# Optimization experiments

Measured on AMD Instinct MI355X. Metric: run time of the kernel, lower is better.

The kernel has to match this reference:

```python
import jax, jax.numpy as jnp
import numpy as np

RADIUS = 0.1
NSAMPLE = 32
NUM_KP = 15
KP_EXTENT = 1.0
DENSITY_PARAM = 5.0
EXTENT = 2.0 * KP_EXTENT * RADIUS / DENSITY_PARAM  # 0.04
K_RADIUS = 1.5 * EXTENT                            # 0.06
C_IN, C_OUT = 64, 128
BN_EPS = 1e-5


def make_kernel_points():
    # Deterministic stand-in for create_kernel_points: first point at center
    # ('center' fixed mode), remaining points quasi-uniform in a ball of K_RADIUS.
    rs = np.random.RandomState(0)
    d = rs.randn(NUM_KP - 1, 3)
    d /= np.linalg.norm(d, axis=1, keepdims=True) + 1e-9
    r = rs.rand(NUM_KP - 1, 1) ** (1.0 / 3.0)
    pts = np.concatenate([np.zeros((1, 3)), d * r * K_RADIUS], axis=0)
    return jnp.asarray(pts, dtype=jnp.float32)  # [K, 3]


def ball_group(query_xyz, support_xyz, support_mask, radius, nsample):
    """Masked ordered ball query. Returns idx [B,N1,S] int32 and mask [B,N1,S] float."""
    # [B, N1, N2] squared distances (dominant memory traffic)
    d2 = jnp.sum((query_xyz[:, :, None, :] - support_xyz[:, None, :, :]) ** 2, axis=-1)
    valid = (d2 < radius * radius) & (support_mask[:, None, :] > 0)
    order = jnp.cumsum(valid.astype(jnp.int32), axis=-1) - 1  # rank among valid, per row
    in_cap = valid & (order < nsample)
    slot = jnp.where(in_cap, order, nsample)  # overflow -> dump slot
    B, N1, N2 = d2.shape
    j = jnp.broadcast_to(jnp.arange(N2, dtype=jnp.int32), (B, N1, N2))
    b = jnp.arange(B)[:, None, None]
    n = jnp.arange(N1)[None, :, None]
    idx = jnp.zeros((B, N1, nsample + 1), jnp.int32).at[b, n, slot].set(j)[..., :nsample]
    cnt = jnp.sum(in_cap.astype(jnp.int32), axis=-1)  # [B, N1]
    nb_mask = jnp.arange(nsample)[None, None, :] < cnt[:, :, None]
    idx = jnp.where(nb_mask, idx, idx[:, :, :1])  # pad with first neighbor
    return idx, nb_mask.astype(jnp.float32)


def setup_inputs() -> dict:
    key = jax.random.key(0)
    ks = jax.random.split(key, 6)
    B, N1, N2 = 4, 2048, 8192
    query_xyz = jax.random.uniform(ks[0], (B, N1, 3), dtype=jnp.float32)
    support_xyz = jax.random.uniform(ks[1], (B, N2, 3), dtype=jnp.float32)
    query_mask = jnp.ones((B, N1), jnp.float32)
    support_mask = jnp.ones((B, N2), jnp.float32)
    support_features = jax.random.normal(ks[2], (B, C_IN, N2), dtype=jnp.float32)
    kernel_weights = jax.random.normal(ks[3], (NUM_KP, C_IN), dtype=jnp.float32) * (1.0 / np.sqrt(C_IN))
    W_out = jax.random.normal(ks[4], (C_OUT, C_IN), dtype=jnp.float32) * (1.0 / np.sqrt(C_IN))
    gamma = jnp.ones((C_OUT,), jnp.float32)
    beta = jnp.zeros((C_OUT,), jnp.float32)
    return {
        "query_xyz": query_xyz, "support_xyz": support_xyz,
        "query_mask": query_mask, "support_mask": support_mask,
        "support_features": support_features, "K_points": make_kernel_points(),
        "kernel_weights": kernel_weights, "W_out": W_out,
        "gamma": gamma, "beta": beta,
    }


def reference(query_xyz, support_xyz, query_mask, support_mask, support_features,
              K_points, kernel_weights, W_out, gamma, beta):
    idx, nb_mask = ball_group(query_xyz, support_xyz, support_mask, RADIUS, NSAMPLE)
    # gather neighbor features: [B, N2, C] -> [B, N1, S, C]
    feats_t = jnp.transpose(support_features, (0, 2, 1))
    nbr_feats = jnp.take_along_axis(feats_t[:, None, :, :],
                                    idx[:, :, :, None], axis=2)  # [B,N1,S,C]
    # grouped relative positions: [B, N1, S, 3]
    grouped_xyz = jnp.take_along_axis(support_xyz[:, None, :, :],
                                      idx[:, :, :, None], axis=2)
    rel_pos = grouped_xyz - query_xyz[:, :, None, :]
    # kernel-point distances: [B, N1, S, K]
    diff = rel_pos[:, :, :, None, :] - K_points[None, None, None, :, :]
    sq_d = jnp.sum(diff * diff, axis=-1)
    # linear influence, then permute to [B, N1, K, S]
    w = jnp.clip(1.0 - jnp.sqrt(sq_d) / EXTENT, 0.0, None)
    w = jnp.transpose(w, (0, 1, 3, 2))
    feature_mask = nb_mask + (1.0 - query_mask[:, :, None])  # [B,N1,S]
    w = w * feature_mask[:, :, None, :]
    # weighted sum over neighbors: [B, N1, K, C]
    weighted = jnp.einsum('bnks,bnsc->bnkc', w, nbr_feats)
    out = jnp.sum(weighted * kernel_weights[None, None, :, :], axis=2)  # [B,N1,C]
    out = jnp.transpose(out, (0, 2, 1))  # [B, C_in, N1]
    # out_conv: 1x1 conv (no bias) + BatchNorm1d (training-mode batch stats) + ReLU
    out = jnp.einsum('oc,bcn->bon', W_out, out)  # [B, C_out, N1]
    mean = jnp.mean(out, axis=(0, 2), keepdims=True)
    var = jnp.mean((out - mean) ** 2, axis=(0, 2), keepdims=True)
    out = (out - mean) * jax.lax.rsqrt(var + BN_EPS)
    out = out * gamma[None, :, None] + beta[None, :, None]
    return jax.nn.relu(out)
```

## Files before the change

kernel.cpp:

```cpp
#include <hip/hip_runtime.h>
#include <stdint.h>
#include <limits.h>

#define BATCH 4
#define N1D   2048
#define N2D   8192
#define NSAMP 32
#define NKP   15
#define CIN   64
#define COUT  128

#define RAD2    0.01f
#define INV_EXT 25.0f
#define BN_EPS  1e-5f
#define CMARG   0.1000001f

#define QPW   1
#define NWAVE 4
#define QPB   (QPW*NWAVE)
#define NCELL 1000
#define MAXC  96

#define WS_PTS4   0
#define WS_BPTS   131072
#define WS_FEATT  262144
#define WS_WT     2359296
#define WS_OUT2   2367488
#define WS_CS     3416064
#define WS_CNT    3420160
#define WS_CUR    3424256

__device__ __forceinline__ int cell_of(float x, float y, float z) {
  int cx = (int)(x*10.f); cx = cx < 0 ? 0 : (cx > 9 ? 9 : cx);
  int cy = (int)(y*10.f); cy = cy < 0 ? 0 : (cy > 9 ? 9 : cy);
  int cz = (int)(z*10.f); cz = cz < 0 ? 0 : (cz > 9 ? 9 : cz);
  return (cx*10 + cy)*10 + cz;
}

__global__ __launch_bounds__(256) void pg_prep(
    const float* __restrict__ sxyz, const float* __restrict__ smask,
    const float* __restrict__ sfeat, const float* __restrict__ Wout,
    float4* __restrict__ pts4, float* __restrict__ featT, float* __restrict__ Wt,
    int* __restrict__ cellCnt)
{
  __shared__ float tile[64*65];
  const int t  = threadIdx.x;
  const int bt = blockIdx.x;

  if (bt == 512) {
#pragma unroll
    for (int i = 0; i < 32; ++i) {
      const int flat = i*256 + t;
      Wt[flat] = Wout[(flat & 127)*CIN + (flat >> 7)];
    }
    return;
  }

  if (bt >= 513) {
    const int idx = bt - 513;
    const int bb  = idx >> 5;
    const int i   = ((idx & 31) << 8) + t;
    if (smask[bb*N2D + i] > 0.f) {
      const float* p = sxyz + ((size_t)bb*N2D + i)*3;
      atomicAdd(&cellCnt[bb*1024 + cell_of(p[0], p[1], p[2])], 1);
    }
    return;
  }

  const int b  = bt >> 7;
  const int j0 = (bt & 127) * 64;
  if (t < 64) {
    const int g = bt*64 + t;
    pts4[g] = make_float4(sxyz[g*3+0], sxyz[g*3+1], sxyz[g*3+2], 0.f);
  }
  const float* src = sfeat + (size_t)(b*CIN)*N2D + j0;
#pragma unroll
  for (int i = 0; i < 4; ++i) {
    const int c  = i*16 + (t >> 4);
    const int j4 = (t & 15) * 4;
    const float4 v = *(const float4*)(src + (size_t)c*N2D + j4);
    tile[c*65 + j4+0] = v.x;
    tile[c*65 + j4+1] = v.y;
    tile[c*65 + j4+2] = v.z;
    tile[c*65 + j4+3] = v.w;
  }
  __syncthreads();
  float* dstb = featT + (size_t)(b*N2D + j0) * CIN;
#pragma unroll
  for (int r = 0; r < 4; ++r) {
    const int j  = r*16 + (t >> 4);
    const int c4 = (t & 15) * 4;
    float4 v;
    v.x = tile[(c4+0)*65 + j];
    v.y = tile[(c4+1)*65 + j];
    v.z = tile[(c4+2)*65 + j];
    v.w = tile[(c4+3)*65 + j];
    *(float4*)(dstb + j*CIN + c4) = v;
  }
}

__global__ __launch_bounds__(256) void pg_scan(
    const int* __restrict__ cellCnt, int* __restrict__ cellStart,
    int* __restrict__ cellCur)
{
  __shared__ int off_s[NCELL+1];
  __shared__ int wsum[4];
  const int t    = threadIdx.x;
  const int lane = t & 63;
  const int wv   = t >> 6;
  const int bb   = blockIdx.x;
  const int* cnt = cellCnt + bb*1024;

  int c0 = 0, c1 = 0, c2 = 0, c3 = 0, v = 0;
  if (t < 250) {
    c0 = cnt[t*4+0]; c1 = cnt[t*4+1]; c2 = cnt[t*4+2]; c3 = cnt[t*4+3];
    v = c0 + c1 + c2 + c3;
  }
  int x = v;
#pragma unroll
  for (int off = 1; off < 64; off <<= 1) {
    int y = __shfl_up(x, off);
    if (lane >= off) x += y;
  }
  if (lane == 63) wsum[wv] = x;
  __syncthreads();
  int base = 0;
#pragma unroll
  for (int w = 0; w < 4; ++w) if (w < wv) base += wsum[w];
  const int excl = base + x - v;
  if (t < 250) {
    int o = excl;
    off_s[t*4+0] = o; o += c0;
    off_s[t*4+1] = o; o += c1;
    off_s[t*4+2] = o; o += c2;
    off_s[t*4+3] = o;
  }
  if (t == 0) off_s[NCELL] = wsum[0]+wsum[1]+wsum[2]+wsum[3];
  __syncthreads();
  for (int i = t; i < NCELL; i += 256) {
    const int o = off_s[i];
    cellStart[bb*(NCELL+1) + i] = o;
    cellCur[bb*1024 + i] = o;
  }
  if (t == 0) cellStart[bb*(NCELL+1) + NCELL] = off_s[NCELL];
}

__global__ __launch_bounds__(256) void pg_scatter(
    const float* __restrict__ sxyz, const float* __restrict__ smask,
    int* __restrict__ cellCur, float4* __restrict__ bpts)
{
  const int idx = blockIdx.x;
  const int bb  = idx >> 5;
  const int i   = ((idx & 31) << 8) + threadIdx.x;
  if (smask[bb*N2D + i] > 0.f) {
    const float* p = sxyz + ((size_t)bb*N2D + i)*3;
    const float px = p[0], py = p[1], pz = p[2];
    const int pos = atomicAdd(&cellCur[bb*1024 + cell_of(px,py,pz)], 1);
    bpts[(size_t)bb*N2D + pos] = make_float4(px, py, pz, __int_as_float(i));
  }
}

__global__ __launch_bounds__(256) void pg_main(
    const float* __restrict__ qxyz, const float* __restrict__ qmask,
    const float4* __restrict__ pts4, const float4* __restrict__ bpts,
    const int* __restrict__ cellStart, const float* __restrict__ featT,
    const float* __restrict__ Kp, const float* __restrict__ KW,
    const float* __restrict__ Wt, float* __restrict__ out2)
{
  __shared__ int      s_segb[QPB][12];
  __shared__ int      s_segc[QPB][12];
  __shared__ int      s_cand[QPB][MAXC];
  __shared__ int      s_idx[QPB*NSAMP];
  __shared__ int      s_cnt[QPB];
  __shared__ float    s_w[QPB*NSAMP*17];
  __shared__ unsigned s_wm[QPB*NSAMP];
  __shared__ float    s_xq[QPB*65];

  const int t    = threadIdx.x;
  const int lane = t & 63;
  const int wv   = t >> 6;
  const int gbase = blockIdx.x * QPB;
  const int b     = gbase >> 11;
  const uint64_t lt = (1ull << lane) - 1ull;

  const float4* bptsb = bpts + (size_t)b*N2D;
  {
    const int ql = wv;
    const int g  = gbase + ql;
    const float qx = qxyz[g*3+0], qy = qxyz[g*3+1], qz = qxyz[g*3+2];
    int cx0 = (int)((qx-CMARG)*10.f); if (cx0 < 0) cx0 = 0;
    int cx1 = (int)((qx+CMARG)*10.f); if (cx1 > 9) cx1 = 9;
    int cy0 = (int)((qy-CMARG)*10.f); if (cy0 < 0) cy0 = 0;
    int cy1 = (int)((qy+CMARG)*10.f); if (cy1 > 9) cy1 = 9;
    int cz0 = (int)((qz-CMARG)*10.f); if (cz0 < 0) cz0 = 0;
    int cz1 = (int)((qz+CMARG)*10.f); if (cz1 > 9) cz1 = 9;
    const int ny = cy1 - cy0 + 1;
    const int npair = (cx1 - cx0 + 1) * ny;

    int len = 0, rs = 0;
    if (lane < npair) {
      const int cx = cx0 + lane / ny;
      const int cy = cy0 + lane % ny;
      const int rowb = (cx*10 + cy)*10;
      const int* csb = cellStart + b*(NCELL+1) + rowb;
      rs = csb[cz0];
      len = csb[cz1 + 1] - rs;
    }
    int c = len;
#pragma unroll
    for (int off = 1; off < 16; off <<= 1) {
      int y = __shfl_up(c, off);
      if (lane >= off) c += y;
    }
    const int tot = __shfl(c, 15);
    const int excl = c - len;
    if (lane < npair) s_segb[ql][lane] = rs - excl;
    if (lane <= npair) s_segc[ql][lane] = excl;

    int ccnt = 0;
    for (int base = 0; base < tot; base += 64) {
      const int idx = base + lane;
      bool ok = false; int jj = 0;
      if (idx < tot) {
        int p = 0;
        while (s_segc[ql][p+1] <= idx) ++p;
        const float4 pt = bptsb[s_segb[ql][p] + idx];
        const float dx = pt.x - qx, dy = pt.y - qy, dz = pt.z - qz;
        ok = (dx*dx + dy*dy + dz*dz) < RAD2;
        jj = __float_as_int(pt.w);
      }
      const uint64_t m = __ballot(ok);
      if (ok) {
        const int pos = ccnt + __popcll(m & lt);
        if (pos < MAXC) s_cand[ql][pos] = jj;
      }
      ccnt += (int)__popcll(m);
    }
    const int C = ccnt < MAXC ? ccnt : MAXC;
    const int C4 = (C + 3) & ~3;
    if (C + lane < C4) s_cand[ql][C + lane] = INT_MAX;

    int jA = (lane      < C) ? s_cand[ql][lane]      : INT_MAX;
    int jB = (lane + 64 < C) ? s_cand[ql][lane + 64] : INT_MAX;
    int rA = 0, rB = 0;
    for (int e = 0; e < C4; e += 4) {
      const int4 v4 = *(const int4*)&s_cand[ql][e];
      rA += (v4.x < jA) + (v4.y < jA) + (v4.z < jA) + (v4.w < jA);
      rB += (v4.x < jB) + (v4.y < jB) + (v4.z < jB) + (v4.w < jB);
    }
    if (lane      < C && rA < NSAMP) s_idx[ql*NSAMP + rA] = jA;
    if (lane + 64 < C && rB < NSAMP) s_idx[ql*NSAMP + rB] = jB;
    if (lane == 0) s_cnt[ql] = C < NSAMP ? C : NSAMP;
  }
  __syncthreads();

  if (t < QPB*NSAMP) {
    const int qslot = t >> 5;
    const int s = t & 31;
    const int c = s_cnt[qslot];
    int j;
    if (s < c) {
      j = s_idx[t];
    } else {
      j = (c > 0) ? s_idx[qslot*NSAMP] : 0;
      s_idx[t] = j;
    }
    const int g = gbase + qslot;
    const float4 pj = pts4[b*N2D + j];
    const float rx = pj.x - qxyz[g*3+0];
    const float ry = pj.y - qxyz[g*3+1];
    const float rz = pj.z - qxyz[g*3+2];

    unsigned msk = 0u;
#pragma unroll
    for (int k = 0; k < NKP; ++k) {
      const float dx = rx - Kp[k*3+0];
      const float dy = ry - Kp[k*3+1];
      const float dz = rz - Kp[k*3+2];
      const float dd = dx*dx + dy*dy + dz*dz;
      const float w = 1.0f - sqrtf(dd) * INV_EXT;
      if (w > 0.0f) {
        s_w[t*17 + k] = w;
        msk |= (1u << k);
      }
    }
    s_wm[t] = msk;
  }
  __syncthreads();

  float kw[NKP];
#pragma unroll
  for (int k = 0; k < NKP; ++k) kw[k] = KW[k*CIN + lane];

  {
    const int ql = wv;
    const int g = gbase + ql;
    const float fpad = 1.0f - qmask[g];
    const int c = __builtin_amdgcn_readfirstlane(s_cnt[ql]);

    float ft[NSAMP];
#pragma unroll
    for (int s = 0; s < NSAMP; ++s) {
      const int j = __builtin_amdgcn_readfirstlane(s_idx[ql*NSAMP + s]);
      ft[s] = featT[(size_t)(b*N2D + j)*CIN + lane];
    }

    float acc = 0.0f;
#pragma unroll
    for (int s = 0; s < NSAMP; ++s) {
      const float fm = ((s < c) ? 1.0f : 0.0f) + fpad;
      if (fm != 0.0f) {
        const unsigned mk =
            (unsigned)__builtin_amdgcn_readfirstlane((int)s_wm[ql*NSAMP + s]);
        if (mk != 0u) {
          const float* wp = &s_w[(ql*NSAMP + s)*17];
          float wsum = 0.0f;
#pragma unroll
          for (int k = 0; k < NKP; ++k)
            if (mk & (1u << k)) wsum += wp[k] * kw[k];
          acc = fmaf(fm*wsum, ft[s], acc);
        }
      }
    }
    s_xq[ql*65 + lane] = acc;
  }
  __syncthreads();

  {
    const int n4 = t & 3;
    const int og = t >> 2;
    const int g  = gbase + n4;
    const int nn = g & 2047;
    float a0 = 0.f, a1 = 0.f;
#pragma unroll
    for (int c = 0; c < CIN; ++c) {
      const float xc = s_xq[n4*65 + c];
      const float2 w2 = *(const float2*)(Wt + c*COUT + og*2);
      a0 = fmaf(w2.x, xc, a0);
      a1 = fmaf(w2.y, xc, a1);
    }
    float* ob = out2 + (size_t)(b*COUT + og*2)*N1D + nn;
    ob[0]   = a0;
    ob[N1D] = a1;
  }
}

__global__ __launch_bounds__(256) void pg_finish(
    const float* __restrict__ out2, const float* __restrict__ gamma,
    const float* __restrict__ beta, float* __restrict__ dout)
{
  __shared__ float red[8];
  __shared__ float mv[2];
  const int t  = threadIdx.x;
  const int o  = blockIdx.x & 127;
  const int bb = blockIdx.x >> 7;
  float4 f[4][2];
  float s1 = 0.f, s2 = 0.f;
#pragma unroll
  for (int r = 0; r < BATCH; ++r) {
    const float4* p = (const float4*)(out2 + (size_t)(r*COUT + o)*N1D);
#pragma unroll
    for (int i = 0; i < 2; ++i) {
      const float4 x = p[i*256 + t];
      f[r][i] = x;
      s1 += x.x + x.y + x.z + x.w;
      s2 += x.x*x.x + x.y*x.y + x.z*x.z + x.w*x.w;
    }
  }
#pragma unroll
  for (int off = 32; off; off >>= 1) {
    s1 += __shfl_xor(s1, off);
    s2 += __shfl_xor(s2, off);
  }
  const int wv = t >> 6;
  if ((t & 63) == 0) { red[wv] = s1; red[4+wv] = s2; }
  __syncthreads();
  if (t == 0) {
    const float inv = 1.0f / (float)(BATCH*N1D);
    const float mean = (red[0]+red[1]+red[2]+red[3]) * inv;
    const float var  = (red[4]+red[5]+red[6]+red[7]) * inv - mean*mean;
    mv[0] = mean;
    mv[1] = rsqrtf(var + BN_EPS);
  }
  __syncthreads();
  const float mean = mv[0];
  const float ga = gamma[o] * mv[1];
  const float be = beta[o];
  float4* dp = (float4*)(dout + (size_t)(bb*COUT + o)*N1D);
#pragma unroll
  for (int i = 0; i < 2; ++i) {
    const float4 x = f[bb][i];
    float4 y;
    y.x = fmaxf((x.x - mean)*ga + be, 0.0f);
    y.y = fmaxf((x.y - mean)*ga + be, 0.0f);
    y.z = fmaxf((x.z - mean)*ga + be, 0.0f);
    y.w = fmaxf((x.w - mean)*ga + be, 0.0f);
    dp[i*256 + t] = y;
  }
}

extern "C" void kernel_launch(void* const* d_in, const int* in_sizes, int n_in,
                              void* d_out, int out_size, void* d_ws, size_t ws_size,
                              hipStream_t stream)
{
  const float* qxyz  = (const float*)d_in[0];
  const float* sxyz  = (const float*)d_in[1];
  const float* qmask = (const float*)d_in[2];
  const float* smask = (const float*)d_in[3];
  const float* sfeat = (const float*)d_in[4];
  const float* Kp    = (const float*)d_in[5];
  const float* KW    = (const float*)d_in[6];
  const float* Wout  = (const float*)d_in[7];
  const float* gamma = (const float*)d_in[8];
  const float* beta  = (const float*)d_in[9];
  float* ws = (float*)d_ws;
  float4* pts4 = (float4*)(ws + WS_PTS4);
  float4* bpts = (float4*)(ws + WS_BPTS);
  float* featT = ws + WS_FEATT;
  float* Wt    = ws + WS_WT;
  float* out2  = ws + WS_OUT2;
  int*   cellS = (int*)(ws + WS_CS);
  int*   cellC = (int*)(ws + WS_CNT);
  int*   cellU = (int*)(ws + WS_CUR);
  float* dst   = (float*)d_out;

  hipMemsetAsync(cellC, 0, BATCH*1024*sizeof(int), stream);
  pg_prep   <<<641,  256, 0, stream>>>(sxyz, smask, sfeat, Wout, pts4, featT,
                                       Wt, cellC);
  pg_scan   <<<4,    256, 0, stream>>>(cellC, cellS, cellU);
  pg_scatter<<<128,  256, 0, stream>>>(sxyz, smask, cellU, bpts);
  pg_main   <<<2048, 256, 0, stream>>>(qxyz, qmask, pts4, bpts, cellS, featT,
                                       Kp, KW, Wt, out2);
  pg_finish <<<512,  256, 0, stream>>>(out2, gamma, beta, dst);
}
```

Before: 144.9 us.

## Make pg_main wave-local, drop block barriers and Wout transpose

Each wave now handles its own query end to end: segment tables live in registers via readlane, and kernel-point weights are computed by the same wave, split across two half-waves. This removes two __syncthreads and the shared count arrays. The separate Wout transpose block in pg_prep is dropped, and the 1x1 conv reads Wout rows directly with float4 loads over padded shared rows. The main risks are higher register pressure and uncoalesced Wout row reads in the conv stage.

```diff
diff --git a/kernel.cpp b/kernel.cpp
--- a/kernel.cpp
+++ b/kernel.cpp
@@ -15,16 +15,14 @@
 #define BN_EPS  1e-5f
 #define CMARG   0.1000001f
 
-#define QPW   1
 #define NWAVE 4
-#define QPB   (QPW*NWAVE)
+#define QPB   NWAVE
 #define NCELL 1000
 #define MAXC  96
 
 #define WS_PTS4   0
 #define WS_BPTS   131072
 #define WS_FEATT  262144
-#define WS_WT     2359296
 #define WS_OUT2   2367488
 #define WS_CS     3416064
 #define WS_CNT    3420160
@@ -39,25 +37,15 @@
 
 __global__ __launch_bounds__(256) void pg_prep(
     const float* __restrict__ sxyz, const float* __restrict__ smask,
-    const float* __restrict__ sfeat, const float* __restrict__ Wout,
-    float4* __restrict__ pts4, float* __restrict__ featT, float* __restrict__ Wt,
-    int* __restrict__ cellCnt)
+    const float* __restrict__ sfeat, float4* __restrict__ pts4,
+    float* __restrict__ featT, int* __restrict__ cellCnt)
 {
   __shared__ float tile[64*65];
   const int t  = threadIdx.x;
   const int bt = blockIdx.x;
 
-  if (bt == 512) {
-#pragma unroll
-    for (int i = 0; i < 32; ++i) {
-      const int flat = i*256 + t;
-      Wt[flat] = Wout[(flat & 127)*CIN + (flat >> 7)];
-    }
-    return;
-  }
-
-  if (bt >= 513) {
-    const int idx = bt - 513;
+  if (bt >= 512) {
+    const int idx = bt - 512;
     const int bb  = idx >> 5;
     const int i   = ((idx & 31) << 8) + t;
     if (smask[bb*N2D + i] > 0.f) {
@@ -165,16 +153,12 @@
     const float4* __restrict__ pts4, const float4* __restrict__ bpts,
     const int* __restrict__ cellStart, const float* __restrict__ featT,
     const float* __restrict__ Kp, const float* __restrict__ KW,
-    const float* __restrict__ Wt, float* __restrict__ out2)
-{
-  __shared__ int      s_segb[QPB][12];
-  __shared__ int      s_segc[QPB][12];
-  __shared__ int      s_cand[QPB][MAXC];
-  __shared__ int      s_idx[QPB*NSAMP];
-  __shared__ int      s_cnt[QPB];
-  __shared__ float    s_w[QPB*NSAMP*17];
-  __shared__ unsigned s_wm[QPB*NSAMP];
-  __shared__ float    s_xq[QPB*65];
+    const float* __restrict__ Wout, float* __restrict__ out2)
+{
+  __shared__ __align__(16) int  s_cand[QPB][MAXC];
+  __shared__ int2               s_im[QPB][NSAMP];
+  __shared__ float              s_w[QPB*NSAMP*17];
+  __shared__ float              s_xq[QPB*68];
 
   const int t    = threadIdx.x;
   const int lane = t & 63;
@@ -183,11 +167,12 @@
   const int b     = gbase >> 11;
   const uint64_t lt = (1ull << lane) - 1ull;
 
+  const int g = gbase + wv;
+  const float qx = qxyz[g*3+0], qy = qxyz[g*3+1], qz = qxyz[g*3+2];
+
   const float4* bptsb = bpts + (size_t)b*N2D;
+  int cq;
   {
-    const int ql = wv;
-    const int g  = gbase + ql;
-    const float qx = qxyz[g*3+0], qy = qxyz[g*3+1], qz = qxyz[g*3+2];
     int cx0 = (int)((qx-CMARG)*10.f); if (cx0 < 0) cx0 = 0;
     int cx1 = (int)((qx+CMARG)*10.f); if (cx1 > 9) cx1 = 9;
     int cy0 = (int)((qy-CMARG)*10.f); if (cy0 < 0) cy0 = 0;
@@ -201,30 +186,38 @@
     if (lane < npair) {
       const int cx = cx0 + lane / ny;
       const int cy = cy0 + lane % ny;
-      const int rowb = (cx*10 + cy)*10;
-      const int* csb = cellStart + b*(NCELL+1) + rowb;
-      rs = csb[cz0];
+      const int* csb = cellStart + b*(NCELL+1) + (cx*10 + cy)*10;
+      rs  = csb[cz0];
       len = csb[cz1 + 1] - rs;
     }
-    int c = len;
+    int pc = len;
 #pragma unroll
     for (int off = 1; off < 16; off <<= 1) {
-      int y = __shfl_up(c, off);
-      if (lane >= off) c += y;
-    }
-    const int tot = __shfl(c, 15);
-    const int excl = c - len;
-    if (lane < npair) s_segb[ql][lane] = rs - excl;
-    if (lane <= npair) s_segc[ql][lane] = excl;
+      int y = __shfl_up(pc, off);
+      if (lane >= off) pc += y;
+    }
+    const int tot   = __shfl(pc, 15);
+    const int excl  = pc - len;
+    const int sbase = rs - excl;
+
+    int segc[9], segb[9];
+#pragma unroll
+    for (int e = 0; e < 9; ++e) {
+      const int ce = __builtin_amdgcn_readlane(excl,  e);
+      const int be = __builtin_amdgcn_readlane(sbase, e);
+      segc[e] = (e < npair) ? ce : INT_MAX;
+      segb[e] = (e < npair) ? be : 0;
+    }
 
     int ccnt = 0;
-    for (int base = 0; base < tot; base += 64) {
-      const int idx = base + lane;
+    for (int base0 = 0; base0 < tot; base0 += 64) {
+      const int idx = base0 + lane;
       bool ok = false; int jj = 0;
       if (idx < tot) {
-        int p = 0;
-        while (s_segc[ql][p+1] <= idx) ++p;
-        const float4 pt = bptsb[s_segb[ql][p] + idx];
+        int bb2 = segb[0];
+#pragma unroll
+        for (int e = 1; e < 9; ++e) if (segc[e] <= idx) bb2 = segb[e];
+        const float4 pt = bptsb[bb2 + idx];
         const float dx = pt.x - qx, dy = pt.y - qy, dz = pt.z - qz;
         ok = (dx*dx + dy*dy + dz*dz) < RAD2;
         jj = __float_as_int(pt.w);
@@ -232,88 +225,84 @@
       const uint64_t m = __ballot(ok);
       if (ok) {
         const int pos = ccnt + __popcll(m & lt);
-        if (pos < MAXC) s_cand[ql][pos] = jj;
+        if (pos < MAXC) s_cand[wv][pos] = jj;
       }
       ccnt += (int)__popcll(m);
     }
     const int C = ccnt < MAXC ? ccnt : MAXC;
     const int C4 = (C + 3) & ~3;
-    if (C + lane < C4) s_cand[ql][C + lane] = INT_MAX;
-
-    int jA = (lane      < C) ? s_cand[ql][lane]      : INT_MAX;
-    int jB = (lane + 64 < C) ? s_cand[ql][lane + 64] : INT_MAX;
+    if (C + lane < C4) s_cand[wv][C + lane] = INT_MAX;
+
+    int jA = (lane      < C) ? s_cand[wv][lane]      : INT_MAX;
+    int jB = (lane + 64 < C) ? s_cand[wv][lane + 64] : INT_MAX;
     int rA = 0, rB = 0;
     for (int e = 0; e < C4; e += 4) {
-      const int4 v4 = *(const int4*)&s_cand[ql][e];
+      const int4 v4 = *(const int4*)&s_cand[wv][e];
       rA += (v4.x < jA) + (v4.y < jA) + (v4.z < jA) + (v4.w < jA);
       rB += (v4.x < jB) + (v4.y < jB) + (v4.z < jB) + (v4.w < jB);
     }
-    if (lane      < C && rA < NSAMP) s_idx[ql*NSAMP + rA] = jA;
-    if (lane + 64 < C && rB < NSAMP) s_idx[ql*NSAMP + rB] = jB;
-    if (lane == 0) s_cnt[ql] = C < NSAMP ? C : NSAMP;
-  }
-  __syncthreads();
-
-  if (t < QPB*NSAMP) {
-    const int qslot = t >> 5;
-    const int s = t & 31;
-    const int c = s_cnt[qslot];
-    int j;
-    if (s < c) {
-      j = s_idx[t];
-    } else {
-      j = (c > 0) ? s_idx[qslot*NSAMP] : 0;
-      s_idx[t] = j;
-    }
-    const int g = gbase + qslot;
+    if (lane      < C && rA < NSAMP) s_im[wv][rA].x = jA;
+    if (lane + 64 < C && rB < NSAMP) s_im[wv][rB].x = jB;
+    cq = C < NSAMP ? C : NSAMP;
+  }
+
+  {
+    const int s    = lane & 31;
+    const int half = lane >> 5;
+    const int raw  = s_im[wv][s].x;
+    const int r0   = s_im[wv][0].x;
+    const int j = (s < cq) ? raw : (cq > 0 ? r0 : 0);
+    if (half == 0) s_im[wv][s].x = j;
+
     const float4 pj = pts4[b*N2D + j];
-    const float rx = pj.x - qxyz[g*3+0];
-    const float ry = pj.y - qxyz[g*3+1];
-    const float rz = pj.z - qxyz[g*3+2];
+    const float rx = pj.x - qx;
+    const float ry = pj.y - qy;
+    const float rz = pj.z - qz;
 
     unsigned msk = 0u;
 #pragma unroll
-    for (int k = 0; k < NKP; ++k) {
-      const float dx = rx - Kp[k*3+0];
-      const float dy = ry - Kp[k*3+1];
-      const float dz = rz - Kp[k*3+2];
-      const float dd = dx*dx + dy*dy + dz*dz;
-      const float w = 1.0f - sqrtf(dd) * INV_EXT;
-      if (w > 0.0f) {
-        s_w[t*17 + k] = w;
-        msk |= (1u << k);
+    for (int ki = 0; ki < 8; ++ki) {
+      const int k = half*8 + ki;
+      if (k < NKP) {
+        const float dx = rx - Kp[k*3+0];
+        const float dy = ry - Kp[k*3+1];
+        const float dz = rz - Kp[k*3+2];
+        const float dd = dx*dx + dy*dy + dz*dz;
+        const float w = 1.0f - sqrtf(dd) * INV_EXT;
+        if (w > 0.0f) {
+          s_w[(wv*NSAMP + s)*17 + k] = w;
+          msk |= (1u << k);
+        }
       }
     }
-    s_wm[t] = msk;
-  }
-  __syncthreads();
-
-  float kw[NKP];
-#pragma unroll
-  for (int k = 0; k < NKP; ++k) kw[k] = KW[k*CIN + lane];
+    msk |= (unsigned)__shfl_xor((int)msk, 32);
+    if (half == 0) s_im[wv][s].y = (int)msk;
+  }
 
   {
-    const int ql = wv;
-    const int g = gbase + ql;
+    float kw[NKP];
+#pragma unroll
+    for (int k = 0; k < NKP; ++k) kw[k] = KW[k*CIN + lane];
+
     const float fpad = 1.0f - qmask[g];
-    const int c = __builtin_amdgcn_readfirstlane(s_cnt[ql]);
+    const int cqs = __builtin_amdgcn_readfirstlane(cq);
 
     float ft[NSAMP];
 #pragma unroll
     for (int s = 0; s < NSAMP; ++s) {
-      const int j = __builtin_amdgcn_readfirstlane(s_idx[ql*NSAMP + s]);
+      const int j = __builtin_amdgcn_readfirstlane(s_im[wv][s].x);
       ft[s] = featT[(size_t)(b*N2D + j)*CIN + lane];
     }
 
     float acc = 0.0f;
 #pragma unroll
     for (int s = 0; s < NSAMP; ++s) {
-      const float fm = ((s < c) ? 1.0f : 0.0f) + fpad;
+      const float fm = ((s < cqs) ? 1.0f : 0.0f) + fpad;
       if (fm != 0.0f) {
         const unsigned mk =
-            (unsigned)__builtin_amdgcn_readfirstlane((int)s_wm[ql*NSAMP + s]);
+            (unsigned)__builtin_amdgcn_readfirstlane(s_im[wv][s].y);
         if (mk != 0u) {
-          const float* wp = &s_w[(ql*NSAMP + s)*17];
+          const float* wp = &s_w[(wv*NSAMP + s)*17];
           float wsum = 0.0f;
 #pragma unroll
           for (int k = 0; k < NKP; ++k)
@@ -322,22 +311,26 @@
         }
       }
     }
-    s_xq[ql*65 + lane] = acc;
+    s_xq[wv*68 + lane] = acc;
   }
   __syncthreads();
 
   {
     const int n4 = t & 3;
     const int og = t >> 2;
-    const int g  = gbase + n4;
-    const int nn = g & 2047;
+    const int gq = gbase + n4;
+    const int nn = gq & 2047;
+    const float4* xr = (const float4*)&s_xq[n4*68];
+    const float4* w0 = (const float4*)(Wout + (og*2+0)*CIN);
+    const float4* w1 = (const float4*)(Wout + (og*2+1)*CIN);
     float a0 = 0.f, a1 = 0.f;
 #pragma unroll
-    for (int c = 0; c < CIN; ++c) {
-      const float xc = s_xq[n4*65 + c];
-      const float2 w2 = *(const float2*)(Wt + c*COUT + og*2);
-      a0 = fmaf(w2.x, xc, a0);
-      a1 = fmaf(w2.y, xc, a1);
+    for (int c4 = 0; c4 < 16; ++c4) {
+      const float4 x4 = xr[c4];
+      const float4 wa = w0[c4];
+      const float4 wb = w1[c4];
+      a0 = fmaf(wa.x, x4.x, fmaf(wa.y, x4.y, fmaf(wa.z, x4.z, fmaf(wa.w, x4.w, a0))));
+      a1 = fmaf(wb.x, x4.x, fmaf(wb.y, x4.y, fmaf(wb.z, x4.z, fmaf(wb.w, x4.w, a1))));
     }
     float* ob = out2 + (size_t)(b*COUT + og*2)*N1D + nn;
     ob[0]   = a0;
@@ -417,7 +410,6 @@
   float4* pts4 = (float4*)(ws + WS_PTS4);
   float4* bpts = (float4*)(ws + WS_BPTS);
   float* featT = ws + WS_FEATT;
-  float* Wt    = ws + WS_WT;
   float* out2  = ws + WS_OUT2;
   int*   cellS = (int*)(ws + WS_CS);
   int*   cellC = (int*)(ws + WS_CNT);
@@ -425,11 +417,10 @@
   float* dst   = (float*)d_out;
 
   hipMemsetAsync(cellC, 0, BATCH*1024*sizeof(int), stream);
-  pg_prep   <<<641,  256, 0, stream>>>(sxyz, smask, sfeat, Wout, pts4, featT,
-                                       Wt, cellC);
+  pg_prep   <<<640,  256, 0, stream>>>(sxyz, smask, sfeat, pts4, featT, cellC);
   pg_scan   <<<4,    256, 0, stream>>>(cellC, cellS, cellU);
   pg_scatter<<<128,  256, 0, stream>>>(sxyz, smask, cellU, bpts);
   pg_main   <<<2048, 256, 0, stream>>>(qxyz, qmask, pts4, bpts, cellS, featT,
-                                       Kp, KW, Wt, out2);
+                                       Kp, KW, Wout, out2);
   pg_finish <<<512,  256, 0, stream>>>(out2, gamma, beta, dst);
 }
```

After: 132.3 us. 8.7% less time.
